# Kernel optimization log

Measured on AMD Instinct MI355X. Metric: run time of the kernel, lower is better.

## Reference

```python
import jax, jax.numpy as jnp
import numpy as np
import math

B, H, S, D = 4, 16, 4096, 128

def setup_inputs() -> dict:
    key = jax.random.key(0)
    kq, kk, kv = jax.random.split(key, 3)
    q = jax.random.normal(kq, (B, H, S, D), dtype=jnp.float32)
    k = jax.random.normal(kk, (B, H, S, D), dtype=jnp.float32)
    v = jax.random.normal(kv, (B, H, S, D), dtype=jnp.float32)
    return {"q": q, "k": k, "v": v}

def reference(q, k, v):
    # Faithful to the torch module: score = (q^T @ k) / sqrt(n_heads)
    # q^T contracts over the SEQUENCE axis -> (B, H, D, D) feature-attention.
    n_heads = q.shape[1]
    scale = 1.0 / math.sqrt(n_heads)
    score = jnp.einsum('bhsd,bhse->bhde', q, k) * scale  # (B,H,D,D)
    score = jax.nn.softmax(score, axis=-1)
    # score @ v^T -> (B,H,D,S)
    out = jnp.einsum('bhde,bhse->bhds', score, v)
    return out
```

## Files before the change

### kernel.cpp

```cpp
#include <hip/hip_runtime.h>

#define BH 64
#define S_ 4096
#define D_ 128
#define SCALE 0.25f

typedef __attribute__((ext_vector_type(4))) short short4v;
typedef __attribute__((ext_vector_type(8))) short short8v;
typedef __attribute__((ext_vector_type(4))) float f32x4;

__device__ inline unsigned short f2bf(float x) {
  union { float f; unsigned u; } v; v.f = x;
  unsigned r = v.u + 0x7fff + ((v.u >> 16) & 1);
  return (unsigned short)(r >> 16);
}
__device__ inline short8v cat8(short4v a, short4v b) {
  short8v r;
  r[0] = a[0]; r[1] = a[1]; r[2] = a[2]; r[3] = a[3];
  r[4] = b[0]; r[5] = b[1]; r[6] = b[2]; r[7] = b[3];
  return r;
}
__device__ inline short4v tr16(unsigned addr) {
  short4v r;
  asm volatile("ds_read_b64_tr_b16 %0, %1" : "=v"(r) : "v"(addr));
  return r;
}
__device__ inline void cvt_pair(float x0, float x1, unsigned& hi, unsigned& lo) {
  unsigned u0 = __float_as_uint(x0), u1 = __float_as_uint(x1);
  unsigned m0 = u0 & 0xffff0000u, m1 = u1 & 0xffff0000u;
  hi = m1 | (u0 >> 16);
  float l0 = x0 - __uint_as_float(m0);
  float l1 = x1 - __uint_as_float(m1);
  lo = (__float_as_uint(l1) & 0xffff0000u) | (__float_as_uint(l0) >> 16);
}
__device__ __forceinline__ void async_copy16(void* lds_dst, const void* g_src) {
  __builtin_amdgcn_global_load_lds(
      (const __attribute__((address_space(1))) void*)g_src,
      (__attribute__((address_space(3))) void*)lds_dst, 16, 0, 0);
}

#define TILE_B2 8192
#define TILE_U2 2048
#define TILE_SH2 4096
#define F_SH 16384
#define F_ROW_F 128

template <int NKS, bool ATOMIC>
__global__ __launch_bounds__(512, 2) void qk_mfma(const float* __restrict__ q,
                                                  const float* __restrict__ k,
                                                  float* __restrict__ part) {
  constexpr int schunk = S_ / NKS;
  constexpr int nsteps = schunk / 32;
  const int bh = blockIdx.x;
  const int ks = blockIdx.y;
  const float* qb = q + (size_t)bh * S_ * D_ + (size_t)ks * schunk * D_;
  const float* kb = k + (size_t)bh * S_ * D_ + (size_t)ks * schunk * D_;

  __shared__ alignas(16) short lds[F_SH + 2 * 8192];
  unsigned* bufU = (unsigned*)&lds[0];
  const unsigned base_u = (unsigned)(uintptr_t)&lds[0];
  float* FQ = (float*)&lds[F_SH];
  float* FK = (float*)&lds[F_SH + 8192];

  const int tid = threadIdx.x;
  const int wv = tid >> 6, lane = tid & 63;
  const int wm = wv & 3;
  const int wn = wv >> 2;

  f32x4 acc[2][4];
#pragma unroll
  for (int a = 0; a < 2; ++a)
#pragma unroll
    for (int b = 0; b < 4; ++b) acc[a][b] = (f32x4){0.f, 0.f, 0.f, 0.f};

  const unsigned lconst = ((unsigned)(lane >> 4) << 10) |
                          ((unsigned)((lane & 15) >> 2) << 5) |
                          ((unsigned)(lane & 3) << 3);
  const unsigned trbase = base_u + lconst;
  const unsigned aQ = trbase;
  const unsigned aK = trbase + 2u * TILE_B2;

  const int row0 = ((tid >> 7) << 2) | ((tid >> 2) & 3);
  const int col0 = (((tid >> 4) & 7) << 4) | ((tid & 3) << 2);

  const int mK = wv >> 2;
  const int w4 = wv & 3;
  const float* matp = mK ? kb : qb;
  short* ldsF = &lds[F_SH + mK * 8192];

  auto dma_step = [&](int st) {
#pragma unroll
    for (int i = 0; i < 4; ++i) {
      const float* src =
          matp + (size_t)(st * 32 + w4 * 8 + i * 2 + (lane >> 5)) * D_ +
          (lane & 31) * 4;
      async_copy16(ldsF + (size_t)(w4 * 4 + i) * 512, src);
    }
  };

  float4 freg[4];
  auto f_read = [&]() {
    freg[0] = *(const float4*)(FQ + row0 * F_ROW_F + col0);
    freg[1] = *(const float4*)(FQ + (row0 + 16) * F_ROW_F + col0);
    freg[2] = *(const float4*)(FK + row0 * F_ROW_F + col0);
    freg[3] = *(const float4*)(FK + (row0 + 16) * F_ROW_F + col0);
  };
  auto cvt_store = [&]() {
#pragma unroll
    for (int i = 0; i < 2; ++i) {
      unsigned off = (unsigned)(tid + i * 512) * 2;
      unsigned h0, l0, h1, l1;
      cvt_pair(freg[i].x, freg[i].y, h0, l0);
      cvt_pair(freg[i].z, freg[i].w, h1, l1);
      *(uint2*)(bufU + off) = make_uint2(h0, h1);
      *(uint2*)(bufU + TILE_U2 + off) = make_uint2(l0, l1);
      cvt_pair(freg[i + 2].x, freg[i + 2].y, h0, l0);
      cvt_pair(freg[i + 2].z, freg[i + 2].w, h1, l1);
      *(uint2*)(bufU + 2 * TILE_U2 + off) = make_uint2(h0, h1);
      *(uint2*)(bufU + 3 * TILE_U2 + off) = make_uint2(l0, l1);
    }
  };

  dma_step(0);
  asm volatile("s_waitcnt vmcnt(0)" ::: "memory");
  __builtin_amdgcn_s_barrier();
  f_read();
  asm volatile("s_waitcnt lgkmcnt(0)" ::: "memory");
  __builtin_amdgcn_sched_barrier(0);
  __builtin_amdgcn_s_barrier();
  if (nsteps > 1) dma_step(1);
  cvt_store();
  asm volatile("s_waitcnt vmcnt(0) lgkmcnt(0)" ::: "memory");
  __builtin_amdgcn_sched_barrier(0);
  __builtin_amdgcn_s_barrier();

  for (int st = 0; st < nsteps; ++st) {
    short4v Bf[4][2][2];
#pragma unroll
    for (int b = 0; b < 4; ++b) {
      unsigned cb = (unsigned)(wn * 4 + b) << 7;
#pragma unroll
      for (int ver = 0; ver < 2; ++ver)
#pragma unroll
        for (int kh = 0; kh < 2; ++kh)
          Bf[b][ver][kh] = tr16(aK + ver * TILE_B2 + kh * 4096 + cb);
    }
    short4v Af[2][2][2];
#pragma unroll
    for (int a = 0; a < 2; ++a) {
      unsigned cb = (unsigned)(wm * 2 + a) << 7;
#pragma unroll
      for (int ver = 0; ver < 2; ++ver)
#pragma unroll
        for (int kh = 0; kh < 2; ++kh)
          Af[a][ver][kh] = tr16(aQ + ver * TILE_B2 + kh * 4096 + cb);
    }
    if (st + 1 < nsteps) f_read();
    asm volatile("s_waitcnt lgkmcnt(0)" ::: "memory");
    __builtin_amdgcn_sched_barrier(0);
    __builtin_amdgcn_s_barrier();

    if (st + 2 < nsteps) dma_step(st + 2);
    if (st + 1 < nsteps) cvt_store();

#pragma unroll
    for (int a = 0; a < 2; ++a) {
      short8v ah = cat8(Af[a][0][0], Af[a][0][1]);
      short8v al = cat8(Af[a][1][0], Af[a][1][1]);
#pragma unroll
      for (int b = 0; b < 4; ++b) {
        short8v bh_ = cat8(Bf[b][0][0], Bf[b][0][1]);
        short8v bl_ = cat8(Bf[b][1][0], Bf[b][1][1]);
        acc[a][b] = __builtin_amdgcn_mfma_f32_16x16x32_bf16(ah, bh_, acc[a][b], 0, 0, 0);
        acc[a][b] = __builtin_amdgcn_mfma_f32_16x16x32_bf16(ah, bl_, acc[a][b], 0, 0, 0);
        acc[a][b] = __builtin_amdgcn_mfma_f32_16x16x32_bf16(al, bh_, acc[a][b], 0, 0, 0);
      }
    }
    asm volatile("s_waitcnt vmcnt(0) lgkmcnt(0)" ::: "memory");
    __builtin_amdgcn_sched_barrier(0);
    __builtin_amdgcn_s_barrier();
  }

  if (!ATOMIC) {
    float* dst = part + ((size_t)ks * BH + bh) * D_ * D_;
#pragma unroll
    for (int a = 0; a < 2; ++a)
#pragma unroll
      for (int b = 0; b < 4; ++b) {
        int e = (wn * 4 + b) * 16 + (lane & 15);
#pragma unroll
        for (int r = 0; r < 4; ++r) {
          int d = (wm * 2 + a) * 16 + ((lane >> 4) << 2) + r;
          dst[(size_t)d * D_ + e] = acc[a][b][r] * SCALE;
        }
      }
  } else {
    float* dst = part + (size_t)bh * D_ * D_;
#pragma unroll
    for (int a = 0; a < 2; ++a)
#pragma unroll
      for (int b = 0; b < 4; ++b) {
        int e = (wn * 4 + b) * 16 + (lane & 15);
#pragma unroll
        for (int r = 0; r < 4; ++r) {
          int d = (wm * 2 + a) * 16 + ((lane >> 4) << 2) + r;
          atomicAdd(&dst[(size_t)d * D_ + e], acc[a][b][r] * SCALE);
        }
      }
  }
}

template <int NKS>
__global__ __launch_bounds__(256) void softmax_k(const float* __restrict__ part,
                                                 short* __restrict__ Pg) {
  const int bh = blockIdx.x;
  const int wv = threadIdx.x >> 6, lane = threadIdx.x & 63;
  const size_t kstride = (size_t)BH * D_ * D_;
  const float* base = part + (size_t)bh * D_ * D_;
  short* dst = Pg + (size_t)bh * D_ * D_;
#pragma unroll
  for (int i = 0; i < 8; ++i) {
    int d = blockIdx.y * 32 + wv * 8 + i;
    float v0 = 0.f, v1 = 0.f;
    for (int ks2 = 0; ks2 < NKS; ++ks2) {
      const float* row = base + ks2 * kstride + (size_t)d * D_;
      v0 += row[lane];
      v1 += row[lane + 64];
    }
    float m = fmaxf(v0, v1);
#pragma unroll
    for (int off = 32; off; off >>= 1) m = fmaxf(m, __shfl_xor(m, off, 64));
    float e0 = __expf(v0 - m), e1 = __expf(v1 - m);
    float s = e0 + e1;
#pragma unroll
    for (int off = 32; off; off >>= 1) s += __shfl_xor(s, off, 64);
    float inv = 1.f / s;
    dst[(size_t)d * D_ + lane] = (short)f2bf(e0 * inv);
    dst[(size_t)d * D_ + lane + 64] = (short)f2bf(e1 * inv);
  }
}

__global__ __launch_bounds__(256) void pv_mfma(const short* __restrict__ Pg,
                                               const float* __restrict__ v,
                                               float* __restrict__ out) {
  const int bh = blockIdx.x;
  const int s0 = blockIdx.y * 128;
  const float* vb = v + (size_t)bh * S_ * D_;
  __shared__ alignas(16) short P_lds[128 * 136];
  __shared__ alignas(16) short V_lds[128 * 36];
  const int tid = threadIdx.x;
  const int wv = tid >> 6, lane = tid & 63;

  const short* Pb = Pg + (size_t)bh * D_ * D_;
#pragma unroll
  for (int i = 0; i < 8; ++i) {
    int idx8 = tid + i * 256;
    int row = idx8 >> 4, c8 = idx8 & 15;
    short8v val = *(const short8v*)(Pb + row * 128 + c8 * 8);
    *(short8v*)(P_lds + row * 136 + c8 * 8) = val;
  }

  f32x4 acc[8][2];
#pragma unroll
  for (int i = 0; i < 8; ++i)
#pragma unroll
    for (int j = 0; j < 2; ++j) acc[i][j] = (f32x4){0.f, 0.f, 0.f, 0.f};

#pragma unroll
  for (int es = 0; es < 4; ++es) {
    __syncthreads();
#pragma unroll
    for (int i = 0; i < 4; ++i) {
      int idx4 = tid + i * 256;
      int s = idx4 >> 3, c4 = idx4 & 7;
      float4 x = *(const float4*)(vb + (size_t)(s0 + s) * D_ + es * 32 + c4 * 4);
      short4v h;
      h[0] = (short)f2bf(x.x); h[1] = (short)f2bf(x.y);
      h[2] = (short)f2bf(x.z); h[3] = (short)f2bf(x.w);
      *(short4v*)(V_lds + s * 36 + c4 * 4) = h;
    }
    __syncthreads();

    short8v a[8];
#pragma unroll
    for (int mt = 0; mt < 8; ++mt) {
      int d = mt * 16 + (lane & 15);
      const short* pr = P_lds + d * 136 + es * 32 + ((lane >> 4) << 2);
      a[mt] = cat8(*(const short4v*)pr, *(const short4v*)(pr + 16));
    }
#pragma unroll
    for (int nl = 0; nl < 2; ++nl) {
      int srow = (wv * 2 + nl) * 16 + (lane & 15);
      const short* vr = V_lds + srow * 36 + ((lane >> 4) << 2);
      short8v b = cat8(*(const short4v*)vr, *(const short4v*)(vr + 16));
#pragma unroll
      for (int mt = 0; mt < 8; ++mt)
        acc[mt][nl] = __builtin_amdgcn_mfma_f32_16x16x32_bf16(a[mt], b, acc[mt][nl], 0, 0, 0);
    }
  }

  float* ob = out + (size_t)bh * D_ * S_ + s0;
#pragma unroll
  for (int mt = 0; mt < 8; ++mt)
#pragma unroll
    for (int nl = 0; nl < 2; ++nl) {
      int sc = (wv * 2 + nl) * 16 + (lane & 15);
#pragma unroll
      for (int r = 0; r < 4; ++r) {
        int d = mt * 16 + ((lane >> 4) << 2) + r;
        ob[(size_t)d * S_ + sc] = acc[mt][nl][r];
      }
    }
}

extern "C" void kernel_launch(void* const* d_in, const int* in_sizes, int n_in,
                              void* d_out, int out_size, void* d_ws,
                              size_t ws_size, hipStream_t stream) {
  const float* q = (const float*)d_in[0];
  const float* k = (const float*)d_in[1];
  const float* v = (const float*)d_in[2];
  float* out = (float*)d_out;
  char* ws = (char*)d_ws;

  const size_t PART1 = (size_t)BH * D_ * D_ * sizeof(float);
  const size_t PSZ = (size_t)BH * D_ * D_ * sizeof(short);

  if (ws_size >= 8 * PART1 + PSZ) {
    float* part = (float*)ws;
    short* Pg = (short*)(ws + 8 * PART1);
    qk_mfma<8, false><<<dim3(BH, 8), 512, 0, stream>>>(q, k, part);
    softmax_k<8><<<dim3(BH, 4), 256, 0, stream>>>(part, Pg);
    pv_mfma<<<dim3(BH, 32), 256, 0, stream>>>(Pg, v, out);
  } else {
    float* part = (float*)ws;
    short* Pg = (short*)(ws + PART1);
    hipMemsetAsync(ws, 0, PART1, stream);
    qk_mfma<16, true><<<dim3(BH, 16), 512, 0, stream>>>(q, k, part);
    softmax_k<1><<<dim3(BH, 4), 256, 0, stream>>>(part, Pg);
    pv_mfma<<<dim3(BH, 32), 256, 0, stream>>>(Pg, v, out);
  }
}
```

Before: 153.4 us.

## Deepen QK fp32 staging into a three-slot async-copy ring with partial waits

Replaces the single fp32 staging buffer in the QK^T kernel with a three-slot LDS ring, prefetching three steps ahead via global_load_lds and waiting only on older loads (vmcnt(4)) instead of draining all outstanding copies each step. This targets global-memory latency that was exposed by the full vmcnt(0) waits. LDS use grows, so launch bounds drop from two blocks per CU to one, which cuts occupancy. The added static_assert requires at least four steps per split.

```diff
diff --git a/kernel.cpp b/kernel.cpp
--- a/kernel.cpp
+++ b/kernel.cpp
@@ -41,26 +41,24 @@
 
 #define TILE_B2 8192
 #define TILE_U2 2048
-#define TILE_SH2 4096
-#define F_SH 16384
-#define F_ROW_F 128
+#define BF16_SH 16384
+#define SLOT_SH 16384
 
 template <int NKS, bool ATOMIC>
-__global__ __launch_bounds__(512, 2) void qk_mfma(const float* __restrict__ q,
+__global__ __launch_bounds__(512, 1) void qk_mfma(const float* __restrict__ q,
                                                   const float* __restrict__ k,
                                                   float* __restrict__ part) {
   constexpr int schunk = S_ / NKS;
   constexpr int nsteps = schunk / 32;
+  static_assert(nsteps >= 4, "ring depth needs >=4 steps");
   const int bh = blockIdx.x;
   const int ks = blockIdx.y;
   const float* qb = q + (size_t)bh * S_ * D_ + (size_t)ks * schunk * D_;
   const float* kb = k + (size_t)bh * S_ * D_ + (size_t)ks * schunk * D_;
 
-  __shared__ alignas(16) short lds[F_SH + 2 * 8192];
+  __shared__ alignas(16) short lds[BF16_SH + 3 * SLOT_SH];
   unsigned* bufU = (unsigned*)&lds[0];
   const unsigned base_u = (unsigned)(uintptr_t)&lds[0];
-  float* FQ = (float*)&lds[F_SH];
-  float* FK = (float*)&lds[F_SH + 8192];
 
   const int tid = threadIdx.x;
   const int wv = tid >> 6, lane = tid & 63;
@@ -86,9 +84,9 @@
   const int mK = wv >> 2;
   const int w4 = wv & 3;
   const float* matp = mK ? kb : qb;
-  short* ldsF = &lds[F_SH + mK * 8192];
-
-  auto dma_step = [&](int st) {
+
+  auto dma_step = [&](int st, int slot) {
+    short* ldsF = &lds[BF16_SH + slot * SLOT_SH + mK * 8192];
 #pragma unroll
     for (int i = 0; i < 4; ++i) {
       const float* src =
@@ -99,11 +97,13 @@
   };
 
   float4 freg[4];
-  auto f_read = [&]() {
-    freg[0] = *(const float4*)(FQ + row0 * F_ROW_F + col0);
-    freg[1] = *(const float4*)(FQ + (row0 + 16) * F_ROW_F + col0);
-    freg[2] = *(const float4*)(FK + row0 * F_ROW_F + col0);
-    freg[3] = *(const float4*)(FK + (row0 + 16) * F_ROW_F + col0);
+  auto f_read = [&](int slot) {
+    const float* FQ = (const float*)&lds[BF16_SH + slot * SLOT_SH];
+    const float* FK = FQ + 4096;
+    freg[0] = *(const float4*)(FQ + row0 * 128 + col0);
+    freg[1] = *(const float4*)(FQ + (row0 + 16) * 128 + col0);
+    freg[2] = *(const float4*)(FK + row0 * 128 + col0);
+    freg[3] = *(const float4*)(FK + (row0 + 16) * 128 + col0);
   };
   auto cvt_store = [&]() {
 #pragma unroll
@@ -121,19 +121,21 @@
     }
   };
 
-  dma_step(0);
-  asm volatile("s_waitcnt vmcnt(0)" ::: "memory");
+  dma_step(0, 0);
+  dma_step(1, 1);
+  dma_step(2, 2);
+  asm volatile("s_waitcnt vmcnt(8)" ::: "memory");
+  __builtin_amdgcn_sched_barrier(0);
   __builtin_amdgcn_s_barrier();
-  f_read();
+  f_read(0);
   asm volatile("s_waitcnt lgkmcnt(0)" ::: "memory");
   __builtin_amdgcn_sched_barrier(0);
-  __builtin_amdgcn_s_barrier();
-  if (nsteps > 1) dma_step(1);
   cvt_store();
-  asm volatile("s_waitcnt vmcnt(0) lgkmcnt(0)" ::: "memory");
+  asm volatile("s_waitcnt vmcnt(4) lgkmcnt(0)" ::: "memory");
   __builtin_amdgcn_sched_barrier(0);
   __builtin_amdgcn_s_barrier();
 
+  int sw = 0;
   for (int st = 0; st < nsteps; ++st) {
     short4v Bf[4][2][2];
 #pragma unroll
@@ -155,12 +157,15 @@
         for (int kh = 0; kh < 2; ++kh)
           Af[a][ver][kh] = tr16(aQ + ver * TILE_B2 + kh * 4096 + cb);
     }
-    if (st + 1 < nsteps) f_read();
+    if (st + 1 < nsteps) {
+      int sr = sw + 1; if (sr == 3) sr = 0;
+      f_read(sr);
+    }
     asm volatile("s_waitcnt lgkmcnt(0)" ::: "memory");
     __builtin_amdgcn_sched_barrier(0);
     __builtin_amdgcn_s_barrier();
 
-    if (st + 2 < nsteps) dma_step(st + 2);
+    if (st + 3 < nsteps) dma_step(st + 3, sw);
     if (st + 1 < nsteps) cvt_store();
 
 #pragma unroll
@@ -176,9 +181,16 @@
         acc[a][b] = __builtin_amdgcn_mfma_f32_16x16x32_bf16(al, bh_, acc[a][b], 0, 0, 0);
       }
     }
-    asm volatile("s_waitcnt vmcnt(0) lgkmcnt(0)" ::: "memory");
+
+    if (st + 4 < nsteps) {
+      asm volatile("s_waitcnt vmcnt(4) lgkmcnt(0)" ::: "memory");
+    } else {
+      asm volatile("s_waitcnt vmcnt(0) lgkmcnt(0)" ::: "memory");
+    }
     __builtin_amdgcn_sched_barrier(0);
     __builtin_amdgcn_s_barrier();
+
+    sw = sw + 1; if (sw == 3) sw = 0;
   }
 
   if (!ATOMIC) {
```

Result: slower. 159.8 us (+4.2%).
